# Kernel tuning notes

Hardware: AMD Instinct MI355X
Metric: run time of the kernel (lower is better)

## Reference

```python
import jax, jax.numpy as jnp
import numpy as np
import math

EMB_DIM = 1024
NUM_HEADS = 16
D_H = EMB_DIM // NUM_HEADS
B, S = 2, 2048


def setup_inputs() -> dict:
    key = jax.random.key(0)
    ks = jax.random.split(key, 6)
    limit = math.sqrt(6.0 / (EMB_DIM + D_H))  # xavier_uniform per head
    x = jax.random.normal(ks[0], (B, S, EMB_DIM), dtype=jnp.float32)
    Wq = jax.random.uniform(ks[1], (NUM_HEADS, EMB_DIM, D_H), jnp.float32, -limit, limit)
    Wk = jax.random.uniform(ks[2], (NUM_HEADS, EMB_DIM, D_H), jnp.float32, -limit, limit)
    Wv = jax.random.uniform(ks[3], (NUM_HEADS, EMB_DIM, D_H), jnp.float32, -limit, limit)
    bq = jnp.zeros((NUM_HEADS, D_H), jnp.float32)
    bk = jnp.zeros((NUM_HEADS, D_H), jnp.float32)
    bv = jnp.zeros((NUM_HEADS, D_H), jnp.float32)
    limo = math.sqrt(6.0 / (EMB_DIM + EMB_DIM))
    W_O = jax.random.uniform(ks[4], (EMB_DIM, EMB_DIM), jnp.float32, -limo, limo)
    causal_mask = jnp.tril(jnp.ones((S, S), jnp.float32))
    padding_mask = jnp.zeros((B, S), jnp.bool_)  # all-False: nothing padded
    return {"x": x, "Wq": Wq, "bq": bq, "Wk": Wk, "bk": bk, "Wv": Wv,
            "bv": bv, "W_O": W_O, "causal_mask": causal_mask,
            "padding_mask": padding_mask}


def reference(x, Wq, bq, Wk, bk, Wv, bv, W_O, causal_mask, padding_mask):
    # Per-head projections, vectorized over heads: [B,S,E] x [H,E,D] -> [B,H,S,D]
    Q = jnp.einsum('bse,hed->bhsd', x, Wq) + bq[None, :, None, :]
    K = jnp.einsum('bse,hed->bhsd', x, Wk) + bk[None, :, None, :]
    V = jnp.einsum('bse,hed->bhsd', x, Wv) + bv[None, :, None, :]
    scores = jnp.einsum('bhsd,bhtd->bhst', Q, K) / math.sqrt(D_H)
    neg_inf = jnp.float32(-jnp.inf)
    scores = jnp.where(causal_mask[None, None, :, :] == 0, neg_inf, scores)
    scores = jnp.where(padding_mask[:, None, None, :], neg_inf, scores)
    attn = jax.nn.softmax(scores, axis=-1)
    out = jnp.einsum('bhst,bhtd->bhsd', attn, V)  # [B,H,S,D]
    # concat heads in order (dim=-1) -> [B,S,H*D]
    x_concat = out.transpose(0, 2, 1, 3).reshape(B, S, EMB_DIM)
    return x_concat @ W_O
```

## Files before the change

### kernel.cpp

```cpp
#include <hip/hip_runtime.h>
#include <hip/hip_bf16.h>


typedef __hip_bfloat16 bf16;
typedef __attribute__((ext_vector_type(8))) short bfrag;
typedef __attribute__((ext_vector_type(4))) float f32x4;
typedef __attribute__((ext_vector_type(16))) float f32x16;
typedef __attribute__((ext_vector_type(4))) short short4v;

#define MFMA16(a, b, c) __builtin_amdgcn_mfma_f32_16x16x32_bf16(a, b, c, 0, 0, 0)
#define MFMA32(a, b, c) __builtin_amdgcn_mfma_f32_32x32x16_bf16(a, b, c, 0, 0, 0)

__device__ __forceinline__ unsigned pk2(float a, float b) {
  union { __hip_bfloat162 h; unsigned u; } w;
  w.h = __float22bfloat162_rn(make_float2(a, b));
  return w.u;
}

__device__ __forceinline__ void gload16(const bf16* g, bf16* l) {
  __builtin_amdgcn_global_load_lds(
      (const __attribute__((address_space(1))) void*)(g),
      (__attribute__((address_space(3))) void*)(l), 16, 0, 0);
}

__device__ __forceinline__ void barrier_raw() {
  asm volatile("" ::: "memory");
  __builtin_amdgcn_s_barrier();
  asm volatile("" ::: "memory");
}

__global__ __launch_bounds__(256) void prep_all(const float* __restrict__ x,
                                                const float* __restrict__ Wq,
                                                const float* __restrict__ Wk,
                                                const float* __restrict__ Wv,
                                                const float* __restrict__ Wo,
                                                bf16* __restrict__ xb,
                                                bf16* __restrict__ WqkvT,
                                                bf16* __restrict__ WoT) {
  __shared__ bf16 tile[64][80];
  int id = blockIdx.x;
  int t = threadIdx.x;
  if (id < 2048) {
    int i = id * 2048 + t * 8;
    float4 a = *(const float4*)(x + i);
    float4 b = *(const float4*)(x + i + 4);
    union { bf16 h[8]; bfrag v; } tmp;
    tmp.h[0] = __float2bfloat16(a.x); tmp.h[1] = __float2bfloat16(a.y);
    tmp.h[2] = __float2bfloat16(a.z); tmp.h[3] = __float2bfloat16(a.w);
    tmp.h[4] = __float2bfloat16(b.x); tmp.h[5] = __float2bfloat16(b.y);
    tmp.h[6] = __float2bfloat16(b.z); tmp.h[7] = __float2bfloat16(b.w);
    *(bfrag*)(xb + i) = tmp.v;
    return;
  }
  int wid = id - 2048;
  const float* src;
  bf16* dst;
  int srcld, dstld, r0, c0;
  if (wid < 768) {
    int w = wid >> 8, h = (wid >> 4) & 15;
    r0 = (wid & 15) * 64; c0 = 0;
    src = ((w == 0) ? Wq : (w == 1) ? Wk : Wv) + (long)h * 1024 * 64;
    dst = WqkvT + ((long)w * 1024 + h * 64) * 1024;
    srcld = 64; dstld = 1024;
  } else {
    int j = wid - 768;
    c0 = (j & 15) * 64; r0 = (j >> 4) * 64;
    src = Wo; dst = WoT;
    srcld = 1024; dstld = 1024;
  }
  int lr = t >> 3, lc = (t & 7) << 3;
#pragma unroll
  for (int p = 0; p < 2; ++p) {
    int r = lr + p * 32;
    const float* s = src + (long)(r0 + r) * srcld + c0 + lc;
    union { bf16 h8[8]; bfrag v; } tmp;
#pragma unroll
    for (int j = 0; j < 8; ++j) tmp.h8[j] = __float2bfloat16(s[j]);
    *(bfrag*)(&tile[r][lc]) = tmp.v;
  }
  __syncthreads();
#pragma unroll
  for (int p = 0; p < 2; ++p) {
    int c = lr + p * 32;
    union { bf16 h8[8]; bfrag v; } tmp;
#pragma unroll
    for (int j = 0; j < 8; ++j) tmp.h8[j] = tile[lc + j][c];
    *(bfrag*)(dst + (long)(c0 + c) * dstld + r0 + lc) = tmp.v;
  }
}

__global__ __launch_bounds__(512, 2) void gemm_qkv128(const bf16* __restrict__ xb,
                                                      const bf16* __restrict__ WT,
                                                      const float* __restrict__ bq,
                                                      const float* __restrict__ bk,
                                                      const float* __restrict__ bv,
                                                      bf16* __restrict__ Q,
                                                      bf16* __restrict__ K_,
                                                      bf16* __restrict__ Vt) {
  extern __shared__ bf16 lds[];
  int id = blockIdx.x;
  int xcd = id & 7, idx = id >> 3;
  int tile = xcd * 24 + idx;
  int mt = tile & 15, nt = tile >> 4;
  int m0 = mt * 256, n0 = nt * 256;

  int t = threadIdx.x;
  int wave = t >> 6, lane = t & 63, quad = lane >> 4, col = lane & 15;
  int wm = wave >> 2, wn = wave & 3;

  int schunk = 8 * ((t & 7) ^ ((t >> 3) & 7));
  const bf16* aSrc = xb + (long)(m0 + (t >> 3)) * 1024 + schunk;
  const bf16* bSrc = WT + (long)(n0 + (t >> 3)) * 1024 + schunk;
  int wv512 = wave * 512;

  int xoff0 = (quad * 8) ^ ((col & 7) << 3);
  const bf16* aRdB = lds + wm * 8192 + col * 64;
  const bf16* bRdB = lds + 32768 + (wn >> 1) * 8192 + (wn & 1) * 4096 + col * 64;

  f32x4 acc[8][4] = {};

#define STA(BUF, HALF, G, KS)                                                  \
  gload16(aSrc + (long)((HALF)*128 + (G)*64) * 1024 + (KS)*64,                 \
          lds + (BUF)*16384 + (HALF)*8192 + (G)*4096 + wv512)
#define STB(BUF, HALF, G, KS)                                                  \
  gload16(bSrc + (long)((HALF)*128 + (G)*64) * 1024 + (KS)*64,                 \
          lds + 32768 + (BUF)*16384 + (HALF)*8192 + (G)*4096 + wv512)

#define PHASE(BUF, MH, KC, STAGES, VMW)                                        \
  {                                                                            \
    int xk = xoff0 ^ ((KC)*32);                                                \
    bfrag ra[4], rb[4];                                                        \
    _Pragma("unroll") for (int u = 0; u < 4; ++u) {                            \
      ra[u] = *(const bfrag*)(aRdB + (BUF)*16384 + (MH)*4096 + u * 1024 + xk); \
      rb[u] = *(const bfrag*)(bRdB + (BUF)*16384 + u * 1024 + xk);             \
    }                                                                          \
    STAGES;                                                                    \
    VMW;                                                                       \
    barrier_raw();                                                             \
    __builtin_amdgcn_s_setprio(1);                                             \
    _Pragma("unroll") for (int ni = 0; ni < 4; ++ni)                           \
      _Pragma("unroll") for (int mi2 = 0; mi2 < 4; ++mi2)                      \
        acc[(MH)*4 + mi2][ni] = MFMA16(ra[mi2], rb[ni], acc[(MH)*4 + mi2][ni]);\
    __builtin_amdgcn_s_setprio(0);                                             \
    barrier_raw();                                                             \
  }

#define VM2 asm volatile("s_waitcnt vmcnt(2)" ::: "memory")
#define NOVM

  STA(0, 0, 0, 0); STA(0, 1, 0, 0); STA(0, 0, 1, 0); STA(0, 1, 1, 0);
  STB(0, 0, 0, 0); STB(0, 0, 1, 0); STB(0, 1, 0, 0); STB(0, 1, 1, 0);
  STA(1, 0, 0, 1); STA(1, 1, 0, 1);
  VM2;
  barrier_raw();

  for (int it = 0; it < 8; ++it) {
    int ksB = 2 * it + 1;
    int kA  = (it < 7) ? 2 * it + 2 : 14;
    int ksB2 = (it < 7) ? 2 * it + 3 : 15;
    PHASE(0, 0, 0, { STA(1, 0, 1, ksB); STA(1, 1, 1, ksB); }, NOVM);
    PHASE(0, 0, 1, { STB(1, 0, 0, ksB); STB(1, 0, 1, ksB); }, NOVM);
    PHASE(0, 1, 0, { STB(1, 1, 0, ksB); STB(1, 1, 1, ksB); }, NOVM);
    PHASE(0, 1, 1, { STA(0, 0, 0, kA); STA(0, 1, 0, kA); }, VM2);
    PHASE(1, 0, 0, { STA(0, 0, 1, kA); STA(0, 1, 1, kA); }, NOVM);
    PHASE(1, 0, 1, { STB(0, 0, 0, kA); STB(0, 0, 1, kA); }, NOVM);
    PHASE(1, 1, 0, { STB(0, 1, 0, kA); STB(0, 1, 1, kA); }, NOVM);
    PHASE(1, 1, 1, { STA(1, 0, 0, ksB2); STA(1, 1, 0, ksB2); }, VM2);
  }
#undef PHASE
#undef STA
#undef STB
#undef VM2
#undef NOVM

  asm volatile("s_waitcnt vmcnt(0)" ::: "memory");
  barrier_raw();

  int sel = n0 >> 10;
  const float* bias = (sel == 0) ? bq : (sel == 1) ? bk : bv;
  float qs = (sel == 0) ? 0.18033688f : 1.0f;
  int b = m0 >> 11, sbase = m0 & 2047, nq = n0 & 1023;
  int seg = (t & 31) * 8;

  if (sel < 2) {
#pragma unroll
    for (int ni = 0; ni < 4; ++ni) {
      int n = wn * 64 + ni * 16 + col;
      float bvv = bias[nq + n];
#pragma unroll
      for (int mi = 0; mi < 8; ++mi) {
        int mrow = wm * 128 + mi * 16 + quad * 4;
#pragma unroll
        for (int r = 0; r < 4; ++r)
          lds[(mrow + r) * 264 + n] = __float2bfloat16((acc[mi][ni][r] + bvv) * qs);
      }
    }
    barrier_raw();
    bf16* dst = (sel == 0) ? Q : K_;
    int h = (nq + seg) >> 6, d = seg & 63;
    long gb = ((long)((b << 4) + h) * 2048 + sbase) * 64 + d;
#pragma unroll
    for (int p = 0; p < 16; ++p) {
      int row = (t >> 5) + p * 16;
      *(bfrag*)(dst + gb + (long)row * 64) = *(const bfrag*)(lds + row * 264 + seg);
    }
  } else {
#pragma unroll
    for (int ni = 0; ni < 4; ++ni) {
      int n = wn * 64 + ni * 16 + col;
      float bvv = bias[nq + n];
#pragma unroll
      for (int mi = 0; mi < 8; ++mi) {
        int m = wm * 128 + mi * 16 + quad * 4;
        union { unsigned u[2]; unsigned long long ull; } pkd;
        pkd.u[0] = pk2(acc[mi][ni][0] + bvv, acc[mi][ni][1] + bvv);
        pkd.u[1] = pk2(acc[mi][ni][2] + bvv, acc[mi][ni][3] + bvv);
        *(unsigned long long*)(lds + n * 264 + m) = pkd.ull;
      }
    }
    barrier_raw();
#pragma unroll
    for (int p = 0; p < 16; ++p) {
      int rn = (t >> 5) + p * 16;
      int h = (nq + rn) >> 6, d = rn & 63;
      *(bfrag*)(Vt + ((long)((b << 4) + h) * 64 + d) * 2048 + sbase + seg) =
          *(const bfrag*)(lds + rn * 264 + seg);
    }
  }
}

__global__ __launch_bounds__(256) void gemm_out(const bf16* __restrict__ O,
                                                const bf16* __restrict__ Bt,
                                                float* __restrict__ Cf) {
  const int K = 1024;
  __shared__ bf16 As[2][128 * 64];
  __shared__ bf16 Bs[2][64 * 64];
  int id = blockIdx.x;
  int xcd = id & 7, sw = id >> 3;
  int m0 = ((xcd << 2) | (sw & 3)) * 128;
  int n0 = (sw >> 2) * 64;
  int t = threadIdx.x;
  int wave = t >> 6, lane = t & 63, quad = lane >> 4, col = lane & 15;
  int wr = (wave >> 1) * 64, wc = (wave & 1) * 32;
  f32x4 acc[2][4] = {};

  int schunk = 8 * ((t & 7) ^ ((t >> 3) & 7));
  int ob = m0 >> 11;
  const bf16* AsrcB = O + (long)ob * 2097152 + (long)((m0 & 2047) + (t >> 3)) * 64 + schunk;
  const bf16* BsrcB = Bt + (long)(n0 + (t >> 3)) * K + schunk;
  int wv = wave * 512;
  int xoff0 = (quad * 8) ^ ((col & 7) << 3);

#define OUT_STAGE(bi, k0n)                                                 \
  {                                                                        \
    long ko = ((long)((k0n) >> 6)) * 131072;                               \
    _Pragma("unroll") for (int i = 0; i < 4; ++i)                          \
      gload16(AsrcB + ko + (long)(32 * i) * 64, &As[bi][i * 2048 + wv]);   \
    _Pragma("unroll") for (int i = 0; i < 2; ++i)                          \
      gload16(BsrcB + (k0n) + (long)(32 * i) * K, &Bs[bi][i * 2048 + wv]); \
  }

  OUT_STAGE(0, 0);
  __syncthreads();
  for (int k0 = 0; k0 < K; k0 += 64) {
    int cur = (k0 >> 6) & 1;
    if (k0 + 64 < K) OUT_STAGE(cur ^ 1, k0 + 64);
#pragma unroll
    for (int kc = 0; kc < 2; ++kc) {
      int xk = xoff0 ^ (kc * 32);
      bfrag ra[4], rb[2];
#pragma unroll
      for (int i = 0; i < 4; ++i)
        ra[i] = *(const bfrag*)(&As[cur][(wr + 16 * i + col) * 64 + xk]);
#pragma unroll
      for (int c = 0; c < 2; ++c)
        rb[c] = *(const bfrag*)(&Bs[cur][(wc + 16 * c + col) * 64 + xk]);
#pragma unroll
      for (int c = 0; c < 2; ++c)
#pragma unroll
        for (int i = 0; i < 4; ++i) acc[c][i] = MFMA16(ra[i], rb[c], acc[c][i]);
    }
    __syncthreads();
  }
#undef OUT_STAGE

#pragma unroll
  for (int c = 0; c < 2; ++c) {
    int n = n0 + wc + 16 * c + col;
#pragma unroll
    for (int i = 0; i < 4; ++i)
#pragma unroll
      for (int r = 0; r < 4; ++r) {
        int m = m0 + wr + 16 * i + quad * 4 + r;
        Cf[(long)m * 1024 + n] = acc[c][i][r];
      }
  }
}

__global__ __launch_bounds__(256) void attn_kernel(const bf16* __restrict__ Q,
                                                   const bf16* __restrict__ K_,
                                                   const bf16* __restrict__ Vt,
                                                   bf16* __restrict__ O) {
  int id = blockIdx.x;
  int xcd = id & 7, jj = id >> 3;
  int qt = 31 - (jj >> 2);
  int bh = ((jj & 3) << 3) | xcd;

  __shared__ bf16 Ks[128][72];
  __shared__ bf16 Vs[64][136];

  int t = threadIdx.x, wave = t >> 6, lane = t & 63;
  int qh = wave >> 1, jh = wave & 1, hi = lane >> 5, l5 = lane & 31;

  int krow = t >> 3, kg = (t & 7) * 8;
  int vrow = t >> 4, vg = (t & 15) * 8;
  const bf16* KuBase = K_ + (long)bh * 2048 * 64;
  const bf16* VuBase = Vt + (long)bh * 64 * 2048;
  int kL = krow * 64 + kg;
  int vL = vrow * 2048 + vg;

  int q0 = qt * 64;
  int nj = (qt >> 1) + 1;
  int qi = q0 + 32 * qh + l5;

  bfrag qa[4];
  const bf16* qp = Q + ((long)bh * 2048 + q0 + 32 * qh + l5) * 64 + hi * 8;
#pragma unroll
  for (int kd = 0; kd < 4; ++kd) qa[kd] = *(const bfrag*)(qp + kd * 16);

  f32x16 o0, o1;
  float lsum = 0.f;
#pragma unroll
  for (int r = 0; r < 16; ++r) { o0[r] = 0.f; o1[r] = 0.f; }

  bfrag kreg[4], vreg[4];
#pragma unroll
  for (int i = 0; i < 4; ++i) {
    kreg[i] = *(const bfrag*)(KuBase + kL + i * 2048);
    vreg[i] = *(const bfrag*)(VuBase + vL + i * 32768);
  }

  for (int jt = 0; jt < nj; ++jt) {
    int j0 = jt * 128;
    __syncthreads();
#pragma unroll
    for (int i = 0; i < 4; ++i) {
      *(bfrag*)(&Ks[krow + 32 * i][kg]) = kreg[i];
      *(bfrag*)(&Vs[vrow + 16 * i][vg]) = vreg[i];
    }
    int jn = (jt + 1 < nj) ? j0 + 128 : j0;
    const bf16* kp = KuBase + (long)jn * 64;
    const bf16* vp = VuBase + jn;
#pragma unroll
    for (int i = 0; i < 4; ++i) {
      kreg[i] = *(const bfrag*)(kp + kL + i * 2048);
      vreg[i] = *(const bfrag*)(vp + vL + i * 32768);
    }
    __syncthreads();

    bool lastT = (jt == nj - 1);
    if (lastT && jh == 1 && ((qt & 1) == 0)) continue;

    f32x16 s0, s1;
#pragma unroll
    for (int r = 0; r < 16; ++r) { s0[r] = 0.f; s1[r] = 0.f; }
    __builtin_amdgcn_s_setprio(1);
#pragma unroll
    for (int kd = 0; kd < 4; ++kd) {
      bfrag ka0 = *(const bfrag*)(&Ks[jh * 64 + l5][kd * 16 + hi * 8]);
      bfrag ka1 = *(const bfrag*)(&Ks[jh * 64 + 32 + l5][kd * 16 + hi * 8]);
      s0 = MFMA32(ka0, qa[kd], s0);
      s1 = MFMA32(ka1, qa[kd], s1);
    }
    __builtin_amdgcn_s_setprio(0);

    unsigned g[2][4][2];
#pragma unroll
    for (int jb = 0; jb < 2; ++jb) {
      float pv[16];
      float ls = 0.f;
#pragma unroll
      for (int r = 0; r < 16; ++r) {
        int jl = (r & 3) + 8 * (r >> 2) + 4 * hi;
        int j = j0 + jh * 64 + jb * 32 + jl;
        float sv = jb ? s1[r] : s0[r];
        float p = __builtin_amdgcn_exp2f(sv);
        if (lastT) p = (j <= qi) ? p : 0.f;
        ls += p;
        pv[r] = p;
      }
      lsum += ls;
#pragma unroll
      for (int gg = 0; gg < 4; ++gg) {
        g[jb][gg][0] = pk2(pv[4 * gg], pv[4 * gg + 1]);
        g[jb][gg][1] = pk2(pv[4 * gg + 2], pv[4 * gg + 3]);
      }
    }

    __builtin_amdgcn_s_setprio(1);
#pragma unroll
    for (int jb = 0; jb < 2; ++jb) {
#pragma unroll
      for (int c = 0; c < 2; ++c) {
        unsigned a0 = g[jb][2 * c][0], a1 = g[jb][2 * c][1];
        unsigned b0 = g[jb][2 * c + 1][0], b1 = g[jb][2 * c + 1][1];
        asm("v_permlane32_swap_b32 %0, %1" : "+v"(a0), "+v"(b0));
        asm("v_permlane32_swap_b32 %0, %1" : "+v"(a1), "+v"(b1));
        union { unsigned u[4]; bfrag f; } pf;
        pf.u[0] = a0;
        pf.u[1] = a1;
        pf.u[2] = b0;
        pf.u[3] = b1;
        int kk = jh * 64 + jb * 32 + c * 16 + hi * 8;
        bfrag av0 = *(const bfrag*)(&Vs[l5][kk]);
        bfrag av1 = *(const bfrag*)(&Vs[32 + l5][kk]);
        o0 = MFMA32(av0, pf.f, o0);
        o1 = MFMA32(av1, pf.f, o1);
      }
    }
    __builtin_amdgcn_s_setprio(0);
  }

  lsum += __shfl_xor(lsum, 32, 64);

  __syncthreads();
  float* Osc = (float*)&Ks[0][0];
  float* Lsc = (float*)&Vs[0][0];
  bf16* Of = (bf16*)((char*)&Vs[0][0] + 512);
  int q = 32 * qh + l5;
  if (jh == 1) {
#pragma unroll
    for (int r = 0; r < 16; ++r) {
      int d = (r & 3) + 8 * (r >> 2) + 4 * hi;
      Osc[q * 68 + d] = o0[r];
      Osc[q * 68 + 32 + d] = o1[r];
    }
    if (hi == 0) Lsc[q] = lsum;
  }
  __syncthreads();
  if (jh == 0) {
    float inv = 1.f / (lsum + Lsc[q]);
#pragma unroll
    for (int r = 0; r < 16; ++r) {
      int d = (r & 3) + 8 * (r >> 2) + 4 * hi;
      Of[q * 72 + d] = __float2bfloat16((o0[r] + Osc[q * 68 + d]) * inv);
      Of[q * 72 + 32 + d] = __float2bfloat16((o1[r] + Osc[q * 68 + 32 + d]) * inv);
    }
  }
  __syncthreads();
  int row = t >> 2, off = (t & 3) * 16;
  bf16* po = O + ((long)bh * 2048 + q0 + row) * 64 + off;
  *(bfrag*)(po) = *(const bfrag*)(&Of[row * 72 + off]);
  *(bfrag*)(po + 8) = *(const bfrag*)(&Of[row * 72 + off + 8]);
}

extern "C" void kernel_launch(void* const* d_in, const int* in_sizes, int n_in,
                              void* d_out, int out_size, void* d_ws, size_t ws_size,
                              hipStream_t stream) {
  const float* x  = (const float*)d_in[0];
  const float* Wq = (const float*)d_in[1];
  const float* bq = (const float*)d_in[2];
  const float* Wk = (const float*)d_in[3];
  const float* bk = (const float*)d_in[4];
  const float* Wv = (const float*)d_in[5];
  const float* bv = (const float*)d_in[6];
  const float* Wo = (const float*)d_in[7];
  float* out = (float*)d_out;

  bf16* ws = (bf16*)d_ws;
  const long MB1 = 1 << 20;
  bf16* WqkvT = ws + 0 * MB1;
  bf16* WoT   = ws + 3 * MB1;
  bf16* Q     = ws + 4 * MB1;
  bf16* K_    = ws + 8 * MB1;
  bf16* Vt    = ws + 12 * MB1;
  bf16* O     = ws + 16 * MB1;
  bf16* xb    = ws + 20 * MB1;

  prep_all<<<3072, 256, 0, stream>>>(x, Wq, Wk, Wv, Wo, xb, WqkvT, WoT);
  gemm_qkv128<<<192, 512, 135168, stream>>>(xb, WqkvT, bq, bk, bv, Q, K_, Vt);
  attn_kernel<<<1024, 256, 0, stream>>>(Q, K_, Vt, O);
  gemm_out<<<512, 256, 0, stream>>>(O, WoT, out);
}
```

Before: 188.2 us.

## Retile QKV GEMM to 256x192 tiles so 256 blocks fill all CUs

The QKV projection GEMM now uses 256x192 output tiles instead of 256x256. That gives 256 workgroups instead of 192, so all 256 CUs on the chip get work and there is no partial wave of blocks. The B-tile staging, LDS layout and accumulator count are reduced to 3 column fragments per wave. The epilogue is rewritten so one tile can straddle the Q/K/V boundary, which needs a special case for the tile at column 1920 that holds both K and V. The trade-offs are lower arithmetic intensity per tile and a more complex epilogue with more branching.

```diff
diff --git a/kernel.cpp b/kernel.cpp
--- a/kernel.cpp
+++ b/kernel.cpp
@@ -100,9 +100,9 @@
   extern __shared__ bf16 lds[];
   int id = blockIdx.x;
   int xcd = id & 7, idx = id >> 3;
-  int tile = xcd * 24 + idx;
+  int tile = xcd * 32 + idx;
   int mt = tile & 15, nt = tile >> 4;
-  int m0 = mt * 256, n0 = nt * 256;
+  int m0 = mt * 256, n0 = nt * 192;
 
   int t = threadIdx.x;
   int wave = t >> 6, lane = t & 63, quad = lane >> 4, col = lane & 15;
@@ -115,30 +115,30 @@
 
   int xoff0 = (quad * 8) ^ ((col & 7) << 3);
   const bf16* aRdB = lds + wm * 8192 + col * 64;
-  const bf16* bRdB = lds + 32768 + (wn >> 1) * 8192 + (wn & 1) * 4096 + col * 64;
-
-  f32x4 acc[8][4] = {};
+  const bf16* bRdB = lds + 32768 + (wn * 48 + col) * 64;
+
+  f32x4 acc[8][3] = {};
 
 #define STA(BUF, HALF, G, KS)                                                  \
   gload16(aSrc + (long)((HALF)*128 + (G)*64) * 1024 + (KS)*64,                 \
           lds + (BUF)*16384 + (HALF)*8192 + (G)*4096 + wv512)
-#define STB(BUF, HALF, G, KS)                                                  \
-  gload16(bSrc + (long)((HALF)*128 + (G)*64) * 1024 + (KS)*64,                 \
-          lds + 32768 + (BUF)*16384 + (HALF)*8192 + (G)*4096 + wv512)
+#define STB(BUF, G, KS)                                                        \
+  gload16(bSrc + (long)((G)*64) * 1024 + (KS)*64,                              \
+          lds + 32768 + (BUF)*12288 + (G)*4096 + wv512)
 
 #define PHASE(BUF, MH, KC, STAGES, VMW)                                        \
   {                                                                            \
     int xk = xoff0 ^ ((KC)*32);                                                \
-    bfrag ra[4], rb[4];                                                        \
-    _Pragma("unroll") for (int u = 0; u < 4; ++u) {                            \
+    bfrag ra[4], rb[3];                                                        \
+    _Pragma("unroll") for (int u = 0; u < 4; ++u)                              \
       ra[u] = *(const bfrag*)(aRdB + (BUF)*16384 + (MH)*4096 + u * 1024 + xk); \
-      rb[u] = *(const bfrag*)(bRdB + (BUF)*16384 + u * 1024 + xk);             \
-    }                                                                          \
+    _Pragma("unroll") for (int c2 = 0; c2 < 3; ++c2)                           \
+      rb[c2] = *(const bfrag*)(bRdB + (BUF)*12288 + c2 * 1024 + xk);           \
     STAGES;                                                                    \
     VMW;                                                                       \
     barrier_raw();                                                             \
     __builtin_amdgcn_s_setprio(1);                                             \
-    _Pragma("unroll") for (int ni = 0; ni < 4; ++ni)                           \
+    _Pragma("unroll") for (int ni = 0; ni < 3; ++ni)                           \
       _Pragma("unroll") for (int mi2 = 0; mi2 < 4; ++mi2)                      \
         acc[(MH)*4 + mi2][ni] = MFMA16(ra[mi2], rb[ni], acc[(MH)*4 + mi2][ni]);\
     __builtin_amdgcn_s_setprio(0);                                             \
@@ -149,7 +149,7 @@
 #define NOVM
 
   STA(0, 0, 0, 0); STA(0, 1, 0, 0); STA(0, 0, 1, 0); STA(0, 1, 1, 0);
-  STB(0, 0, 0, 0); STB(0, 0, 1, 0); STB(0, 1, 0, 0); STB(0, 1, 1, 0);
+  STB(0, 0, 0); STB(0, 1, 0); STB(0, 2, 0);
   STA(1, 0, 0, 1); STA(1, 1, 0, 1);
   VM2;
   barrier_raw();
@@ -159,12 +159,12 @@
     int kA  = (it < 7) ? 2 * it + 2 : 14;
     int ksB2 = (it < 7) ? 2 * it + 3 : 15;
     PHASE(0, 0, 0, { STA(1, 0, 1, ksB); STA(1, 1, 1, ksB); }, NOVM);
-    PHASE(0, 0, 1, { STB(1, 0, 0, ksB); STB(1, 0, 1, ksB); }, NOVM);
-    PHASE(0, 1, 0, { STB(1, 1, 0, ksB); STB(1, 1, 1, ksB); }, NOVM);
+    PHASE(0, 0, 1, { STB(1, 0, ksB); STB(1, 1, ksB); }, NOVM);
+    PHASE(0, 1, 0, { STB(1, 2, ksB); }, NOVM);
     PHASE(0, 1, 1, { STA(0, 0, 0, kA); STA(0, 1, 0, kA); }, VM2);
     PHASE(1, 0, 0, { STA(0, 0, 1, kA); STA(0, 1, 1, kA); }, NOVM);
-    PHASE(1, 0, 1, { STB(0, 0, 0, kA); STB(0, 0, 1, kA); }, NOVM);
-    PHASE(1, 1, 0, { STB(0, 1, 0, kA); STB(0, 1, 1, kA); }, NOVM);
+    PHASE(1, 0, 1, { STB(0, 0, kA); STB(0, 1, kA); }, NOVM);
+    PHASE(1, 1, 0, { STB(0, 2, kA); }, NOVM);
     PHASE(1, 1, 1, { STA(1, 0, 0, ksB2); STA(1, 1, 0, ksB2); }, VM2);
   }
 #undef PHASE
@@ -176,39 +176,89 @@
   asm volatile("s_waitcnt vmcnt(0)" ::: "memory");
   barrier_raw();
 
-  int sel = n0 >> 10;
-  const float* bias = (sel == 0) ? bq : (sel == 1) ? bk : bv;
-  float qs = (sel == 0) ? 0.18033688f : 1.0f;
-  int b = m0 >> 11, sbase = m0 & 2047, nq = n0 & 1023;
-  int seg = (t & 31) * 8;
-
-  if (sel < 2) {
-#pragma unroll
-    for (int ni = 0; ni < 4; ++ni) {
-      int n = wn * 64 + ni * 16 + col;
-      float bvv = bias[nq + n];
+  const float SC2 = 0.18033688f;
+  int b = m0 >> 11, sbase = m0 & 2047;
+
+  if (n0 < 1920) {
+#pragma unroll
+    for (int ni = 0; ni < 3; ++ni) {
+      int n = wn * 48 + ni * 16 + col;
+      int ng = n0 + n;
+      int s01 = ng >> 10;
+      float bvv = s01 ? bk[ng & 1023] : bq[ng & 1023];
+      float qsv = s01 ? 1.0f : SC2;
 #pragma unroll
       for (int mi = 0; mi < 8; ++mi) {
         int mrow = wm * 128 + mi * 16 + quad * 4;
 #pragma unroll
         for (int r = 0; r < 4; ++r)
-          lds[(mrow + r) * 264 + n] = __float2bfloat16((acc[mi][ni][r] + bvv) * qs);
+          lds[(mrow + r) * 200 + n] = __float2bfloat16((acc[mi][ni][r] + bvv) * qsv);
       }
     }
     barrier_raw();
-    bf16* dst = (sel == 0) ? Q : K_;
-    int h = (nq + seg) >> 6, d = seg & 63;
-    long gb = ((long)((b << 4) + h) * 2048 + sbase) * 64 + d;
-#pragma unroll
-    for (int p = 0; p < 16; ++p) {
-      int row = (t >> 5) + p * 16;
-      *(bfrag*)(dst + gb + (long)row * 64) = *(const bfrag*)(lds + row * 264 + seg);
+    int row = t >> 1, half = t & 1;
+#pragma unroll
+    for (int s = 0; s < 12; ++s) {
+      int cl = 96 * half + 8 * s;
+      int ng = n0 + cl;
+      int s01 = ng >> 10, within = ng & 1023;
+      int h = within >> 6, d = within & 63;
+      bf16* dst = s01 ? K_ : Q;
+      *(bfrag*)(dst + ((long)((b << 4) + h) * 2048 + sbase + row) * 64 + d) =
+          *(const bfrag*)(lds + row * 200 + cl);
+    }
+  } else if (n0 == 1920) {
+#pragma unroll
+    for (int ni = 0; ni < 3; ++ni) {
+      int n = wn * 48 + ni * 16 + col;
+      int ng = n0 + n;
+      if (ng < 2048) {
+        float bvv = bk[ng & 1023];
+#pragma unroll
+        for (int mi = 0; mi < 8; ++mi) {
+          int mrow = wm * 128 + mi * 16 + quad * 4;
+#pragma unroll
+          for (int r = 0; r < 4; ++r)
+            lds[(mrow + r) * 136 + n] = __float2bfloat16(acc[mi][ni][r] + bvv);
+        }
+      } else {
+        int vn = n - 128;
+        float bvv = bv[ng & 1023];
+#pragma unroll
+        for (int mi = 0; mi < 8; ++mi) {
+          int m = wm * 128 + mi * 16 + quad * 4;
+          union { unsigned u[2]; unsigned long long ull; } pkd;
+          pkd.u[0] = pk2(acc[mi][ni][0] + bvv, acc[mi][ni][1] + bvv);
+          pkd.u[1] = pk2(acc[mi][ni][2] + bvv, acc[mi][ni][3] + bvv);
+          *(unsigned long long*)(lds + 34816 + vn * 264 + m) = pkd.ull;
+        }
+      }
+    }
+    barrier_raw();
+#pragma unroll
+    for (int p = 0; p < 8; ++p) {
+      int u = p * 512 + t;
+      int row = u >> 4, cl = (u & 15) * 8;
+      int within = (n0 + cl) & 1023;
+      int h = within >> 6, d = within & 63;
+      *(bfrag*)(K_ + ((long)((b << 4) + h) * 2048 + sbase + row) * 64 + d) =
+          *(const bfrag*)(lds + row * 136 + cl);
+    }
+#pragma unroll
+    for (int p = 0; p < 4; ++p) {
+      int u = p * 512 + t;
+      int vn = u >> 5, seg = (u & 31) * 8;
+      int within = (n0 + 128 + vn) & 1023;
+      int h = within >> 6, d = within & 63;
+      *(bfrag*)(Vt + ((long)((b << 4) + h) * 64 + d) * 2048 + sbase + seg) =
+          *(const bfrag*)(lds + 34816 + vn * 264 + seg);
     }
   } else {
 #pragma unroll
-    for (int ni = 0; ni < 4; ++ni) {
-      int n = wn * 64 + ni * 16 + col;
-      float bvv = bias[nq + n];
+    for (int ni = 0; ni < 3; ++ni) {
+      int n = wn * 48 + ni * 16 + col;
+      int ng = n0 + n;
+      float bvv = bv[ng & 1023];
 #pragma unroll
       for (int mi = 0; mi < 8; ++mi) {
         int m = wm * 128 + mi * 16 + quad * 4;
@@ -220,9 +270,11 @@
     }
     barrier_raw();
 #pragma unroll
-    for (int p = 0; p < 16; ++p) {
-      int rn = (t >> 5) + p * 16;
-      int h = (nq + rn) >> 6, d = rn & 63;
+    for (int p = 0; p < 12; ++p) {
+      int u = p * 512 + t;
+      int rn = u >> 5, seg = (u & 31) * 8;
+      int within = (n0 + rn) & 1023;
+      int h = within >> 6, d = within & 63;
       *(bfrag*)(Vt + ((long)((b << 4) + h) * 64 + d) * 2048 + sbase + seg) =
           *(const bfrag*)(lds + rn * 264 + seg);
     }
@@ -478,7 +530,7 @@
   bf16* xb    = ws + 20 * MB1;
 
   prep_all<<<3072, 256, 0, stream>>>(x, Wq, Wk, Wv, Wo, xb, WqkvT, WoT);
-  gemm_qkv128<<<192, 512, 135168, stream>>>(xb, WqkvT, bq, bk, bv, Q, K_, Vt);
+  gemm_qkv128<<<256, 512, 114688, stream>>>(xb, WqkvT, bq, bk, bv, Q, K_, Vt);
   attn_kernel<<<1024, 256, 0, stream>>>(Q, K_, Vt, O);
   gemm_out<<<512, 256, 0, stream>>>(O, WoT, out);
 }
```

New measurement: 186.4 us. About the same (-1.0%).
